# Kernel optimization log

Hardware: AMD Instinct MI355X
Metric: run time of the kernel (lower is better)

The kernel has to match this reference:

```python
import jax, jax.numpy as jnp
import numpy as np

N_NODES = 100000
N_EDGES = 1600000
D_IN = 128
D_OUT = 128


def setup_inputs() -> dict:
    key = jax.random.key(0)
    k1, k2, k3, k4, k5 = jax.random.split(key, 5)
    H = jax.random.normal(k1, (N_NODES, D_IN), dtype=jnp.float32)
    vals = jax.random.uniform(k2, (N_EDGES,), dtype=jnp.float32)
    W = jax.random.normal(k3, (D_OUT, D_IN), dtype=jnp.float32) * (1.0 / np.sqrt(D_IN))
    rows = jax.random.randint(k4, (N_EDGES,), 0, N_NODES, dtype=jnp.int32)
    cols = jax.random.randint(k5, (N_EDGES,), 0, N_NODES, dtype=jnp.int32)
    return {"H": H, "vals": vals, "W": W, "rows": rows, "cols": cols}


def reference(H, vals, W, rows, cols):
    # Single-rank: communicate_fgm is a no-op (X is zeros, no remote peers).
    # SpMM: out[i] = sum_e vals[e] * H[cols[e]] for edges with rows[e] == i
    msgs = vals[:, None] * H[cols]                      # [n_edges, d_in] irregular gather
    AH = jax.ops.segment_sum(msgs, rows, num_segments=N_NODES)  # [n_nodes, d_in]
    # Linear (no bias) + ReLU
    out = jax.nn.relu(AH @ W.T)                          # [n_nodes, d_out]
    return out
```

## Files before the change

### kernel.cpp

```cpp
#include <hip/hip_runtime.h>

#define N_NODES 100000
#define N_EDGES 1600000
#define D 128
#define CAPR 48
#define NTILES 6250

#define NTHR 256
#define NBA 320
#define CHUNKA 5000
#define NGB 1563
#define NSUP 196
#define SLOTA 8960
#define SLOTH 4608
#define NTHR3 512

#define WB_OFF    0u
#define HWB_OFF   65536u
#define SCNTA_OFF 25665536u

typedef unsigned int uint;
typedef __attribute__((ext_vector_type(4))) float f32x4;
typedef __attribute__((ext_vector_type(4))) uint  u32x4;
typedef __attribute__((ext_vector_type(2))) uint  u32x2;
typedef __attribute__((ext_vector_type(2))) int   i32x2;
typedef __attribute__((ext_vector_type(8))) short bf16x8;

__device__ __forceinline__ unsigned short f2bf(float x) {
    uint u = __float_as_uint(x);
    uint r = u + 0x7fffu + ((u >> 16) & 1u);
    return (unsigned short)(r >> 16);
}

__device__ __forceinline__ void acc8(float acc[8], u32x4 q, float v) {
    acc[0] = fmaf(v, __uint_as_float(q.x << 16),         acc[0]);
    acc[1] = fmaf(v, __uint_as_float(q.x & 0xffff0000u), acc[1]);
    acc[2] = fmaf(v, __uint_as_float(q.y << 16),         acc[2]);
    acc[3] = fmaf(v, __uint_as_float(q.y & 0xffff0000u), acc[3]);
    acc[4] = fmaf(v, __uint_as_float(q.z << 16),         acc[4]);
    acc[5] = fmaf(v, __uint_as_float(q.z & 0xffff0000u), acc[5]);
    acc[6] = fmaf(v, __uint_as_float(q.w << 16),         acc[6]);
    acc[7] = fmaf(v, __uint_as_float(q.w & 0xffff0000u), acc[7]);
}

__global__ __launch_bounds__(NTHR) void k_cast(const float* __restrict__ W,
                                               unsigned short* __restrict__ Wb,
                                               int* __restrict__ scntA) {
    int b = blockIdx.x;
    if (b < 64) {
        int i = b * NTHR + threadIdx.x;
        Wb[i] = f2bf(W[i]);
    } else {
        if (threadIdx.x < NSUP) scntA[threadIdx.x] = 0;
    }
}

__global__ __launch_bounds__(NTHR) void k_gemm_bucketA(
        const float* __restrict__ H, const unsigned short* __restrict__ Wb,
        unsigned short* __restrict__ HWb, const int* __restrict__ rows,
        const int* __restrict__ cols, const float* __restrict__ vals,
        int* __restrict__ scntA, i32x2* __restrict__ epackA) {
    const int bid = blockIdx.x;
    const int tid = threadIdx.x;

    if (bid < NBA) {
        __shared__ int hist[NSUP];
        __shared__ int cur[NSUP];
        const int e0 = bid * CHUNKA;

        if (tid < NSUP) hist[tid] = 0;
        __syncthreads();
        for (int i = tid; i < CHUNKA; i += NTHR)
            atomicAdd(&hist[rows[e0 + i] >> 9], 1);
        __syncthreads();
        if (tid < NSUP) {
            int c = hist[tid];
            int base = (c > 0) ? atomicAdd(&scntA[tid], c) : 0;
            cur[tid] = tid * SLOTA + base;
        }
        __syncthreads();
        for (int i = tid; i < CHUNKA; i += NTHR) {
            int r = rows[e0 + i];
            int s = r >> 9;
            int p = atomicAdd(&cur[s], 1);
            if (p < (s + 1) * SLOTA)
                epackA[p] = (i32x2){((r & 511) << 17) | cols[e0 + i],
                                    __float_as_int(vals[e0 + i])};
        }
        return;
    }

    const int wave = tid >> 6;
    const int lane = tid & 63;
    const int rowtile = (bid - NBA) * 4 + wave;
    if (rowtile >= NTILES) return;
    const int rowbase = rowtile * 16;
    const int m    = lane & 15;
    const int quad = lane >> 4;

    f32x4 acc[8];
    #pragma unroll
    for (int nt = 0; nt < 8; ++nt) acc[nt] = (f32x4){0.f, 0.f, 0.f, 0.f};

    const float* hrow = H + (size_t)(rowbase + m) * D;
    #pragma unroll
    for (int ks = 0; ks < 4; ++ks) {
        const int k0 = ks * 32 + quad * 8;
        f32x4 a0 = __builtin_nontemporal_load((const f32x4*)(hrow + k0));
        f32x4 a1 = __builtin_nontemporal_load((const f32x4*)(hrow + k0 + 4));
        bf16x8 hfr;
        hfr[0] = (short)f2bf(a0.x); hfr[1] = (short)f2bf(a0.y);
        hfr[2] = (short)f2bf(a0.z); hfr[3] = (short)f2bf(a0.w);
        hfr[4] = (short)f2bf(a1.x); hfr[5] = (short)f2bf(a1.y);
        hfr[6] = (short)f2bf(a1.z); hfr[7] = (short)f2bf(a1.w);
        #pragma unroll
        for (int nt = 0; nt < 8; ++nt) {
            bf16x8 wfr = *(const bf16x8*)(Wb + (size_t)(nt * 16 + m) * D + k0);
            acc[nt] = __builtin_amdgcn_mfma_f32_16x16x32_bf16(wfr, hfr, acc[nt], 0, 0, 0);
        }
    }

    unsigned short* orow = HWb + (size_t)(rowbase + m) * D;
    #pragma unroll
    for (int nt = 0; nt < 8; ++nt) {
        u32x2 o;
        o.x = (uint)f2bf(acc[nt][0]) | ((uint)f2bf(acc[nt][1]) << 16);
        o.y = (uint)f2bf(acc[nt][2]) | ((uint)f2bf(acc[nt][3]) << 16);
        *(u32x2*)(orow + nt * 16 + quad * 4) = o;
    }
}

__global__ __launch_bounds__(NTHR3) void k_spmm_hs(
        const int* __restrict__ scntA, const i32x2* __restrict__ epackA,
        const unsigned short* __restrict__ HWb, float* __restrict__ out) {
    __shared__ i32x2 eq[SLOTH];
    __shared__ i32x2 sE[32][CAPR + 1];
    __shared__ int   cnt[32];
    __shared__ int   qn;
    const int tid = threadIdx.x;
    const int s   = blockIdx.x >> 1;
    const int hh  = blockIdx.x & 1;
    const int n   = min(scntA[s], SLOTA);
    const i32x2* src = epackA + (size_t)s * SLOTA;

    if (tid == 0) qn = 0;
    __syncthreads();
    for (int i = tid; i < n; i += NTHR3) {
        i32x2 e  = __builtin_nontemporal_load(&src[i]);
        int   lr = e.x >> 17;
        if ((lr >> 8) == hh) {
            int k = atomicAdd(&qn, 1);
            if (k < SLOTH)
                eq[k] = (i32x2){((lr & 255) << 17) | (e.x & 0x1FFFF), e.y};
        }
    }
    __syncthreads();

    const int ne      = min(qn, SLOTH);
    const int rowbase = (s << 9) + (hh << 8);
    const int lane    = tid & 15;
    const int group   = tid >> 4;

    for (int c = 0; c < 8; ++c) {
        if (tid < 32) cnt[tid] = 0;
        __syncthreads();
        for (int i = tid; i < ne; i += NTHR3) {
            i32x2 e  = eq[i];
            int   lr = e.x >> 17;
            if ((lr >> 5) == c) {
                int k = atomicAdd(&cnt[lr & 31], 1);
                if (k < CAPR) sE[lr & 31][k] = (i32x2){e.x & 0x1FFFF, e.y};
            }
        }
        __syncthreads();

        const int row = rowbase + (c << 5) + group;
        if (row < N_NODES) {
            const int e_ = min(cnt[group], CAPR);
            float acc[8];
            #pragma unroll
            for (int k = 0; k < 8; ++k) acc[k] = 0.f;

            int j = 0;
            for (; j + 3 < e_; j += 4) {
                i32x2 e0 = sE[group][j],     e1 = sE[group][j + 1];
                i32x2 e2 = sE[group][j + 2], e3 = sE[group][j + 3];
                u32x4 q0 = ((const u32x4*)(HWb + (size_t)e0.x * D))[lane];
                u32x4 q1 = ((const u32x4*)(HWb + (size_t)e1.x * D))[lane];
                u32x4 q2 = ((const u32x4*)(HWb + (size_t)e2.x * D))[lane];
                u32x4 q3 = ((const u32x4*)(HWb + (size_t)e3.x * D))[lane];
                acc8(acc, q0, __int_as_float(e0.y));
                acc8(acc, q1, __int_as_float(e1.y));
                acc8(acc, q2, __int_as_float(e2.y));
                acc8(acc, q3, __int_as_float(e3.y));
            }
            for (; j < e_; ++j) {
                i32x2 e = sE[group][j];
                u32x4 q = ((const u32x4*)(HWb + (size_t)e.x * D))[lane];
                acc8(acc, q, __int_as_float(e.y));
            }

            f32x4 o0 = (f32x4){fmaxf(acc[0], 0.f), fmaxf(acc[1], 0.f),
                               fmaxf(acc[2], 0.f), fmaxf(acc[3], 0.f)};
            f32x4 o1 = (f32x4){fmaxf(acc[4], 0.f), fmaxf(acc[5], 0.f),
                               fmaxf(acc[6], 0.f), fmaxf(acc[7], 0.f)};
            __builtin_nontemporal_store(o0, &((f32x4*)out)[row * 32 + lane * 2]);
            __builtin_nontemporal_store(o1, &((f32x4*)out)[row * 32 + lane * 2 + 1]);
        }
        __syncthreads();
    }
}

extern "C" void kernel_launch(void* const* d_in, const int* in_sizes, int n_in,
                              void* d_out, int out_size, void* d_ws, size_t ws_size,
                              hipStream_t stream) {
    const float* H    = (const float*)d_in[0];
    const float* vals = (const float*)d_in[1];
    const float* W    = (const float*)d_in[2];
    const int*   rows = (const int*)d_in[3];
    const int*   cols = (const int*)d_in[4];
    float* out = (float*)d_out;

    char* ws = (char*)d_ws;
    unsigned short* Wb     = (unsigned short*)(ws + WB_OFF);
    unsigned short* HWb    = (unsigned short*)(ws + HWB_OFF);
    int*            scntA  = (int*)(ws + SCNTA_OFF);
    i32x2*          epackA = (i32x2*)d_out;

    k_cast<<<65, NTHR, 0, stream>>>(W, Wb, scntA);

    k_gemm_bucketA<<<NBA + NGB, NTHR, 0, stream>>>(H, Wb, HWb, rows, cols,
                                                   vals, scntA, epackA);

    k_spmm_hs<<<2 * NSUP, NTHR3, 0, stream>>>(scntA, epackA, HWb, out);
}
```

Before: 228.7 us.

## Replace global-atomic edge buckets with fixed per-block cells and fold W cast into GEMM

Drops the separate cast/zero-init kernel. W is now converted to bf16 inline inside the GEMM tiles. Edge bucketing no longer uses global atomics on per-supertile counters: each bucketing block writes into its own fixed-size cell per supertile and records the count there. The edge chunk per block is halved so there are twice as many cells. The SpMM kernel gathers from the 640 small cells per supertile using 16-lane groups, which trades contiguous reads for many short scattered ones. It also repeats the W conversion in every GEMM tile and silently drops edges if a cell overflows its 38-entry capacity.

```diff
diff --git a/kernel.cpp b/kernel.cpp
--- a/kernel.cpp
+++ b/kernel.cpp
@@ -7,17 +7,16 @@
 #define NTILES 6250
 
 #define NTHR 256
-#define NBA 320
-#define CHUNKA 5000
+#define NBA 640
+#define CHUNKA 2500
 #define NGB 1563
 #define NSUP 196
-#define SLOTA 8960
+#define EPC 38
 #define SLOTH 4608
 #define NTHR3 512
 
-#define WB_OFF    0u
-#define HWB_OFF   65536u
-#define SCNTA_OFF 25665536u
+#define HWB_OFF 0u
+#define BCOUNT_OFF_IN_OUT 38133760u
 
 typedef unsigned int uint;
 typedef __attribute__((ext_vector_type(4))) float f32x4;
@@ -43,23 +42,11 @@
     acc[7] = fmaf(v, __uint_as_float(q.w & 0xffff0000u), acc[7]);
 }
 
-__global__ __launch_bounds__(NTHR) void k_cast(const float* __restrict__ W,
-                                               unsigned short* __restrict__ Wb,
-                                               int* __restrict__ scntA) {
-    int b = blockIdx.x;
-    if (b < 64) {
-        int i = b * NTHR + threadIdx.x;
-        Wb[i] = f2bf(W[i]);
-    } else {
-        if (threadIdx.x < NSUP) scntA[threadIdx.x] = 0;
-    }
-}
-
-__global__ __launch_bounds__(NTHR) void k_gemm_bucketA(
-        const float* __restrict__ H, const unsigned short* __restrict__ Wb,
+__global__ __launch_bounds__(NTHR) void k_gemm_bucket(
+        const float* __restrict__ H, const float* __restrict__ W,
         unsigned short* __restrict__ HWb, const int* __restrict__ rows,
         const int* __restrict__ cols, const float* __restrict__ vals,
-        int* __restrict__ scntA, i32x2* __restrict__ epackA) {
+        i32x2* __restrict__ epackA, int* __restrict__ bcount) {
     const int bid = blockIdx.x;
     const int tid = threadIdx.x;
 
@@ -74,16 +61,16 @@
             atomicAdd(&hist[rows[e0 + i] >> 9], 1);
         __syncthreads();
         if (tid < NSUP) {
-            int c = hist[tid];
-            int base = (c > 0) ? atomicAdd(&scntA[tid], c) : 0;
-            cur[tid] = tid * SLOTA + base;
+            int cell = tid * NBA + bid;
+            cur[tid] = cell * EPC;
+            bcount[cell] = min(hist[tid], EPC);
         }
         __syncthreads();
         for (int i = tid; i < CHUNKA; i += NTHR) {
             int r = rows[e0 + i];
             int s = r >> 9;
             int p = atomicAdd(&cur[s], 1);
-            if (p < (s + 1) * SLOTA)
+            if (p < (s * NBA + bid) * EPC + EPC)
                 epackA[p] = (i32x2){((r & 511) << 17) | cols[e0 + i],
                                     __float_as_int(vals[e0 + i])};
         }
@@ -115,7 +102,14 @@
         hfr[6] = (short)f2bf(a1.z); hfr[7] = (short)f2bf(a1.w);
         #pragma unroll
         for (int nt = 0; nt < 8; ++nt) {
-            bf16x8 wfr = *(const bf16x8*)(Wb + (size_t)(nt * 16 + m) * D + k0);
+            const float* wrow = W + (size_t)(nt * 16 + m) * D + k0;
+            f32x4 w0 = *(const f32x4*)(wrow);
+            f32x4 w1 = *(const f32x4*)(wrow + 4);
+            bf16x8 wfr;
+            wfr[0] = (short)f2bf(w0.x); wfr[1] = (short)f2bf(w0.y);
+            wfr[2] = (short)f2bf(w0.z); wfr[3] = (short)f2bf(w0.w);
+            wfr[4] = (short)f2bf(w1.x); wfr[5] = (short)f2bf(w1.y);
+            wfr[6] = (short)f2bf(w1.z); wfr[7] = (short)f2bf(w1.w);
             acc[nt] = __builtin_amdgcn_mfma_f32_16x16x32_bf16(wfr, hfr, acc[nt], 0, 0, 0);
         }
     }
@@ -130,36 +124,40 @@
     }
 }
 
-__global__ __launch_bounds__(NTHR3) void k_spmm_hs(
-        const int* __restrict__ scntA, const i32x2* __restrict__ epackA,
+__global__ __launch_bounds__(NTHR3) void k_spmm_cells(
+        const i32x2* __restrict__ epackA, const int* __restrict__ bcount,
         const unsigned short* __restrict__ HWb, float* __restrict__ out) {
     __shared__ i32x2 eq[SLOTH];
     __shared__ i32x2 sE[32][CAPR + 1];
     __shared__ int   cnt[32];
     __shared__ int   qn;
-    const int tid = threadIdx.x;
-    const int s   = blockIdx.x >> 1;
-    const int hh  = blockIdx.x & 1;
-    const int n   = min(scntA[s], SLOTA);
-    const i32x2* src = epackA + (size_t)s * SLOTA;
+    const int tid   = threadIdx.x;
+    const int s     = blockIdx.x >> 1;
+    const int hh    = blockIdx.x & 1;
+    const int lane  = tid & 15;
+    const int group = tid >> 4;
 
     if (tid == 0) qn = 0;
     __syncthreads();
-    for (int i = tid; i < n; i += NTHR3) {
-        i32x2 e  = __builtin_nontemporal_load(&src[i]);
-        int   lr = e.x >> 17;
-        if ((lr >> 8) == hh) {
-            int k = atomicAdd(&qn, 1);
-            if (k < SLOTH)
-                eq[k] = (i32x2){((lr & 255) << 17) | (e.x & 0x1FFFF), e.y};
+
+    for (int b = group; b < NBA; b += 32) {
+        const int idx = s * NBA + b;
+        const int n   = bcount[idx];
+        const i32x2* src = epackA + (size_t)idx * EPC;
+        for (int i = lane; i < n; i += 16) {
+            i32x2 e  = src[i];
+            int   lr = e.x >> 17;
+            if ((lr >> 8) == hh) {
+                int k = atomicAdd(&qn, 1);
+                if (k < SLOTH)
+                    eq[k] = (i32x2){((lr & 255) << 17) | (e.x & 0x1FFFF), e.y};
+            }
         }
     }
     __syncthreads();
 
     const int ne      = min(qn, SLOTH);
     const int rowbase = (s << 9) + (hh << 8);
-    const int lane    = tid & 15;
-    const int group   = tid >> 4;
 
     for (int c = 0; c < 8; ++c) {
         if (tid < 32) cnt[tid] = 0;
@@ -221,16 +219,12 @@
     const int*   cols = (const int*)d_in[4];
     float* out = (float*)d_out;
 
-    char* ws = (char*)d_ws;
-    unsigned short* Wb     = (unsigned short*)(ws + WB_OFF);
-    unsigned short* HWb    = (unsigned short*)(ws + HWB_OFF);
-    int*            scntA  = (int*)(ws + SCNTA_OFF);
+    unsigned short* HWb    = (unsigned short*)((char*)d_ws + HWB_OFF);
     i32x2*          epackA = (i32x2*)d_out;
-
-    k_cast<<<65, NTHR, 0, stream>>>(W, Wb, scntA);
-
-    k_gemm_bucketA<<<NBA + NGB, NTHR, 0, stream>>>(H, Wb, HWb, rows, cols,
-                                                   vals, scntA, epackA);
-
-    k_spmm_hs<<<2 * NSUP, NTHR3, 0, stream>>>(scntA, epackA, HWb, out);
-}
+    int*            bcount = (int*)((char*)d_out + BCOUNT_OFF_IN_OUT);
+
+    k_gemm_bucket<<<NBA + NGB, NTHR, 0, stream>>>(H, W, HWb, rows, cols, vals,
+                                                  epackA, bcount);
+
+    k_spmm_cells<<<2 * NSUP, NTHR3, 0, stream>>>(epackA, bcount, HWb, out);
+}
```

After: 264.8 us. +15.8%, slower.
